# Optimization experiments

Hardware: AMD Instinct MI355X
Metric: run time of the kernel (lower is better)

## Reference

```python
import jax, jax.numpy as jnp
import numpy as np

NUM_ITEMS = 50000
B = 512      # batch of (user, item) pairs
L = 50       # padded per-user item-list length
K = 20       # top_k: length of each context channel
H = 32       # hidden_dim
D = 32       # output_dim


def setup_inputs() -> dict:
    key = jax.random.key(0)
    ks = jax.random.split(key, 8)
    ctx = jax.random.normal(ks[0], (NUM_ITEMS, 10, K), dtype=jnp.float32)
    item_idxs = jax.random.randint(ks[1], (B,), 0, NUM_ITEMS)
    user_items = jax.random.randint(ks[2], (B, L), 0, NUM_ITEMS)
    user_lens = jax.random.randint(ks[3], (B,), 1, L + 1)  # ragged lengths in [1, L]
    W1 = jax.random.normal(ks[4], (5, 1, H), dtype=jnp.float32) * 0.1
    b1 = jnp.zeros((5, H), dtype=jnp.float32)
    W2 = jax.random.normal(ks[5], (5, H, D), dtype=jnp.float32) * 0.1
    b2 = jnp.zeros((5, D), dtype=jnp.float32)
    Wout = jax.random.normal(ks[6], (D, 1), dtype=jnp.float32) * 0.1
    bout = jnp.zeros((1,), dtype=jnp.float32)
    return dict(ctx=ctx, W1=W1, b1=b1, W2=W2, b2=b2, Wout=Wout, bout=bout,
                item_idxs=item_idxs, user_items=user_items, user_lens=user_lens)


def _item_rep(feat, W1, b1, W2, b2):
    """feat: [..., 10, K] context channels -> [..., 5*K, D] item representation.
    Channels (2c, 2c+1) go through com_{c+1}: a shared 1->H->D MLP applied to each
    scalar (unsqueeze(1) in the original), outputs of the two channels multiplied."""
    prefix = feat.shape[:-2]
    x = feat.reshape(prefix + (5, 2, K))                     # [..., 5, 2, K]
    w1 = W1[:, 0, :].reshape((5, 1, 1, H))                   # input_dim == 1
    h = jax.nn.relu(x[..., None] * w1 + b1.reshape((5, 1, 1, H)))   # [..., 5, 2, K, H]
    o = jnp.einsum('...cpkh,chd->...cpkd', h, W2) + b2.reshape((5, 1, 1, D))
    rep = o[..., 0, :, :] * o[..., 1, :, :]                  # [..., 5, K, D]
    return rep.reshape(prefix + (5 * K, D))


def reference(ctx, W1, b1, W2, b2, Wout, bout, item_idxs, user_items, user_lens):
    # Target-item representations: gather contexts then tiny MLPs. [B, 5K, D]
    item_rep = _item_rep(ctx[item_idxs], W1, b1, W2, b2)
    # Per-user item reps (padded ragged) and masked mean over the item list.
    u_rep = _item_rep(ctx[user_items], W1, b1, W2, b2)       # [B, L, 5K, D]
    mask = (jnp.arange(L)[None, :] < user_lens[:, None]).astype(u_rep.dtype)  # [B, L]
    u_mean = jnp.einsum('blnd,bl->bnd', u_rep, mask) / user_lens[:, None, None].astype(u_rep.dtype)
    inter = u_mean * item_rep                                # [B, 5K, D]
    pred = jax.nn.sigmoid(inter @ Wout + bout)               # [B, 5K, 1]
    return pred.reshape(B * 5 * K, 1)
```

## Files before the change

kernel.cpp:

```cpp
#include <hip/hip_runtime.h>
#include <math.h>

#define NITEMS 50000
#define BATCH  512
#define LLEN   50
#define KTOP   20
#define HDIM   32
#define DDIM   32
#define NCH    5
#define NSEG   33
#define NSCAL  200
#define NCELL  100
#define THRP   33
#define NWAVE  8
#define CSLOT  13

typedef _Float16 h2 __attribute__((ext_vector_type(2)));

static __device__ __forceinline__ float dot2_acc(h2 a, h2 b, float c) {
#if __has_builtin(__builtin_amdgcn_fdot2)
    return __builtin_amdgcn_fdot2(a, b, c, false);
#else
    return fmaf((float)a.x, (float)b.x, fmaf((float)a.y, (float)b.y, c));
#endif
}

#define WS_THRS  0
#define WS_AB16  160
#define WS_ORDER 5440


__global__ __launch_bounds__(256) void cnn_setup(
        const float* __restrict__ W1, const float* __restrict__ b1,
        const float* __restrict__ W2, const float* __restrict__ b2,
        const int* __restrict__ user_lens,
        float* __restrict__ ws, int* __restrict__ order) {
    const int tid = threadIdx.x;

    if (blockIdx.x < NSEG) {
        __shared__ float sW1[NCH*HDIM], sB1[NCH*HDIM], sThr[NCH*HDIM];
        __shared__ int   sRank[NCH*HDIM];
        __shared__ float sW2[NCH*HDIM*DDIM];
        __shared__ float sB2[NCH*DDIM];

        for (int i = tid; i < NCH*HDIM; i += 256) { sW1[i] = W1[i]; sB1[i] = b1[i]; }
        for (int i = tid; i < NCH*HDIM*DDIM; i += 256) sW2[i] = W2[i];
        for (int i = tid; i < NCH*DDIM; i += 256) sB2[i] = b2[i];
        __syncthreads();

        for (int i = tid; i < NCH*HDIM; i += 256) {
            float w = sW1[i];
            sThr[i] = (w != 0.f) ? (-sB1[i] / w) : INFINITY;
        }
        __syncthreads();

        for (int i = tid; i < NCH*HDIM; i += 256) {
            int c = i / HDIM, h = i % HDIM;
            float thr = sThr[i];
            int rank = 0;
            for (int h2i = 0; h2i < HDIM; ++h2i) {
                float thr2 = sThr[c*HDIM + h2i];
                rank += (thr2 < thr || (thr2 == thr && h2i < h)) ? 1 : 0;
            }
            sRank[i] = rank;
            if (blockIdx.x == 0) ws[WS_THRS + c*HDIM + rank] = thr;
        }
        __syncthreads();

        const int s = blockIdx.x;
        if (tid < NCH*DDIM) {
            int c = tid / DDIM, d = tid % DDIM;
            float A = 0.f, Bv = 0.f;
#pragma unroll
            for (int h = 0; h < HDIM; ++h) {
                float w  = sW1[c*HDIM + h];
                float bb = sB1[c*HDIM + h];
                int   r  = sRank[c*HDIM + h];
                bool active = (w > 0.f) ? (r < s) : ((w < 0.f) ? (r >= s) : (bb > 0.f));
                if (active) {
                    float w2 = sW2[(c*HDIM + h)*DDIM + d];
                    A  = fmaf(w,  w2, A);
                    Bv = fmaf(bb, w2, Bv);
                }
            }
            Bv += sB2[c*DDIM + d];
            unsigned short* ab = (unsigned short*)(ws + WS_AB16);
            int d4 = d >> 2, dd = d & 3;
            int base = ((c*NSEG + s)*32 + d4*4)*2;
            _Float16 ah = (_Float16)A, bh = (_Float16)Bv;
            ab[base + 4*(dd>>1) + (dd&1)]     = __builtin_bit_cast(unsigned short, ah);
            ab[base + 4*(dd>>1) + 2 + (dd&1)] = __builtin_bit_cast(unsigned short, bh);
        }
    } else {
        __shared__ int k512[BATCH], v512[BATCH];
        for (int i = tid; i < BATCH; i += 256) { k512[i] = user_lens[i]; v512[i] = i; }
        __syncthreads();
        for (int k = 2; k <= BATCH; k <<= 1) {
            for (int j = k >> 1; j > 0; j >>= 1) {
                int i   = ((tid & ~(j - 1)) << 1) | (tid & (j - 1));
                int ixj = i | j;
                bool up = ((i & k) == 0);
                int ka = k512[i], kb = k512[ixj];
                if ((ka > kb) == up) {
                    k512[i] = kb; k512[ixj] = ka;
                    int va = v512[i]; v512[i] = v512[ixj]; v512[ixj] = va;
                }
                __syncthreads();
            }
        }
        for (int i = tid; i < BATCH; i += 256) order[i] = v512[i];
    }
}

__global__ __launch_bounds__(512, 4) void cnn_main(
        const float* __restrict__ ctx,  const float* __restrict__ ws,
        const float* __restrict__ Wout, const float* __restrict__ bout,
        const int* __restrict__ item_idxs, const int* __restrict__ user_items,
        const int* __restrict__ user_lens, const int* __restrict__ order,
        float* __restrict__ out) {
    __shared__ unsigned int sAB16[NCH*NSEG*32];
    __shared__ float  sThrS[NCH*THRP];
    __shared__ float4 sxo[NWAVE][NCELL];
    __shared__ union WScr {
        float rawx[NSCAL];
        float pRed[NCELL];
    } wscr[NWAVE];

    const int tid  = threadIdx.x;
    const int w    = tid >> 6;
    const int lane = tid & 63;
    const int g    = lane >> 3;
    const int d4   = lane & 7;

    const uint4* ABg = reinterpret_cast<const uint4*>(ws + WS_AB16);
    uint4* sAB4 = reinterpret_cast<uint4*>(sAB16);
    for (int i = tid; i < NCH*NSEG*8; i += 512) sAB4[i] = ABg[i];
    for (int i = tid; i < NCH*THRP; i += 512) {
        int c = i / THRP, j = i - c*THRP;
        sThrS[i] = (j < HDIM) ? ws[WS_THRS + c*HDIM + j] : 0.f;
    }

    const int rank = (blockIdx.x < 256) ? blockIdx.x : (767 - blockIdx.x);
    const int b    = order[rank];
    const int len  = user_lens[b];
    const float inv_len = 1.f / (float)len;
    const float bo = bout[0];
    const h2 wv0 = {(_Float16)Wout[4*d4],     (_Float16)Wout[4*d4 + 1]};
    const h2 wv1 = {(_Float16)Wout[4*d4 + 2], (_Float16)Wout[4*d4 + 3]};

    int sc[4], sdx[4], sdo[4];
#pragma unroll
    for (int r = 0; r < 4; ++r) {
        int idx  = lane + 64*r;
        int c    = idx / 40, rr = idx - c*40;
        int cell = c*KTOP + (rr % KTOP);
        int p    = rr / KTOP;
        sc[r]  = c;
        sdx[r] = cell*16 + p*4;
        sdo[r] = cell*16 + 8 + p*2;
    }

    const int nstripe = (len > w) ? ((len - w + NWAVE - 1) / NWAVE) : 0;

    unsigned int wtA[CSLOT], wtB[CSLOT];
    float acc[CSLOT];
#pragma unroll
    for (int i = 0; i < CSLOT; ++i) acc[i] = 0.f;

    __syncthreads();

    char* sxoB = (char*)&sxo[w][0];

    float4 x4 = make_float4(0.f, 0.f, 0.f, 0.f);
    {
        int it0 = item_idxs[b];
        if (lane < 50) x4 = *((const float4*)(ctx + (size_t)it0*NSCAL) + lane);
    }
    if (lane < 50) *((float4*)&wscr[w].rawx[0] + lane) = x4;
    __builtin_amdgcn_wave_barrier();

#pragma unroll
    for (int r = 0; r < 4; ++r) {
        int idx = lane + 64*r;
        if (idx < NSCAL) {
            float xv = wscr[w].rawx[idx];
            int base = sc[r]*THRP;
            int pos = 0;
            pos += (sThrS[base + pos + 15] < xv) ? 16 : 0;
            pos += (sThrS[base + pos + 7]  < xv) ? 8  : 0;
            pos += (sThrS[base + pos + 3]  < xv) ? 4  : 0;
            pos += (sThrS[base + pos + 1]  < xv) ? 2  : 0;
            pos += (sThrS[base + pos]      < xv) ? 1  : 0;
            int off = (sc[r]*NSEG + pos) << 7;
            *(float*)(sxoB + sdx[r]) = xv;
            *(unsigned short*)(sxoB + sdo[r]) = (unsigned short)off;
        }
    }
    __builtin_amdgcn_wave_barrier();

    float4 xn4 = make_float4(0.f, 0.f, 0.f, 0.f);
    if (nstripe > 0) {
        int nit = user_items[b*LLEN + w];
        if (lane < 50) xn4 = *((const float4*)(ctx + (size_t)nit*NSCAL) + lane);
    }

#pragma unroll
    for (int i = 0; i < CSLOT; ++i) {
        int cell = g + 8*i;
        if (cell < NCELL) {
            float4 xo = sxo[w][cell];
            unsigned int offs = __builtin_bit_cast(unsigned int, xo.z);
            const uint4* p0 = (const uint4*)((const char*)sAB16 + (offs & 0xffffu) + (d4 << 4));
            const uint4* p1 = (const uint4*)((const char*)sAB16 + (offs >> 16)     + (d4 << 4));
            uint4 q0 = *p0, q1 = *p1;
            _Float16 x0h = (_Float16)xo.x, x1h = (_Float16)xo.y;
            h2 x0 = {x0h, x0h}, x1 = {x1h, x1h};
            h2 repa = (x0 * __builtin_bit_cast(h2, q0.x) + __builtin_bit_cast(h2, q0.y))
                    * (x1 * __builtin_bit_cast(h2, q1.x) + __builtin_bit_cast(h2, q1.y));
            h2 repb = (x0 * __builtin_bit_cast(h2, q0.z) + __builtin_bit_cast(h2, q0.w))
                    * (x1 * __builtin_bit_cast(h2, q1.z) + __builtin_bit_cast(h2, q1.w));
            wtA[i] = __builtin_bit_cast(unsigned int, (h2)(repa * wv0));
            wtB[i] = __builtin_bit_cast(unsigned int, (h2)(repb * wv1));
        }
    }
    __builtin_amdgcn_wave_barrier();
    x4 = xn4;

    for (int j = 0; j < nstripe; ++j) {
        if (lane < 50) *((float4*)&wscr[w].rawx[0] + lane) = x4;
        __builtin_amdgcn_wave_barrier();

        xn4 = make_float4(0.f, 0.f, 0.f, 0.f);
        if (j + 1 < nstripe) {
            int nit = user_items[b*LLEN + w + NWAVE*(j + 1)];
            if (lane < 50) xn4 = *((const float4*)(ctx + (size_t)nit*NSCAL) + lane);
        }

#pragma unroll
        for (int r = 0; r < 4; ++r) {
            int idx = lane + 64*r;
            if (idx < NSCAL) {
                float xv = wscr[w].rawx[idx];
                int base = sc[r]*THRP;
                int pos = 0;
                pos += (sThrS[base + pos + 15] < xv) ? 16 : 0;
                pos += (sThrS[base + pos + 7]  < xv) ? 8  : 0;
                pos += (sThrS[base + pos + 3]  < xv) ? 4  : 0;
                pos += (sThrS[base + pos + 1]  < xv) ? 2  : 0;
                pos += (sThrS[base + pos]      < xv) ? 1  : 0;
                int off = (sc[r]*NSEG + pos) << 7;
                *(float*)(sxoB + sdx[r]) = xv;
                *(unsigned short*)(sxoB + sdo[r]) = (unsigned short)off;
            }
        }
        __builtin_amdgcn_wave_barrier();

#pragma unroll
        for (int i = 0; i < CSLOT; ++i) {
            int cell = g + 8*i;
            if (cell < NCELL) {
                float4 xo = sxo[w][cell];
                unsigned int offs = __builtin_bit_cast(unsigned int, xo.z);
                const uint4* p0 = (const uint4*)((const char*)sAB16 + (offs & 0xffffu) + (d4 << 4));
                const uint4* p1 = (const uint4*)((const char*)sAB16 + (offs >> 16)     + (d4 << 4));
                uint4 q0 = *p0, q1 = *p1;
                _Float16 x0h = (_Float16)xo.x, x1h = (_Float16)xo.y;
                h2 x0 = {x0h, x0h}, x1 = {x1h, x1h};
                h2 repa = (x0 * __builtin_bit_cast(h2, q0.x) + __builtin_bit_cast(h2, q0.y))
                        * (x1 * __builtin_bit_cast(h2, q1.x) + __builtin_bit_cast(h2, q1.y));
                h2 repb = (x0 * __builtin_bit_cast(h2, q0.z) + __builtin_bit_cast(h2, q0.w))
                        * (x1 * __builtin_bit_cast(h2, q1.z) + __builtin_bit_cast(h2, q1.w));
                acc[i] = dot2_acc(repa, __builtin_bit_cast(h2, wtA[i]),
                         dot2_acc(repb, __builtin_bit_cast(h2, wtB[i]), acc[i]));
            }
        }
        __builtin_amdgcn_wave_barrier();
        x4 = xn4;
    }

#pragma unroll
    for (int i = 0; i < CSLOT; ++i) {
        int cell = g + 8*i;
        float v = acc[i];
        v += __shfl_xor(v, 1, 64);
        v += __shfl_xor(v, 2, 64);
        v += __shfl_xor(v, 4, 64);
        if (d4 == 0 && cell < NCELL) wscr[w].pRed[cell] = v;
    }
    __syncthreads();
    if (tid < NCELL) {
        float p = 0.f;
#pragma unroll
        for (int q = 0; q < NWAVE; ++q) p += wscr[q].pRed[tid];
        out[b*NCELL + tid] = 1.f / (1.f + expf(-(p*inv_len + bo)));
    }
}

extern "C" void kernel_launch(void* const* d_in, const int* in_sizes, int n_in,
                              void* d_out, int out_size, void* d_ws, size_t ws_size,
                              hipStream_t stream) {
    const float* ctx   = (const float*)d_in[0];
    const float* W1    = (const float*)d_in[1];
    const float* b1    = (const float*)d_in[2];
    const float* W2    = (const float*)d_in[3];
    const float* b2    = (const float*)d_in[4];
    const float* Wout  = (const float*)d_in[5];
    const float* bout  = (const float*)d_in[6];
    const int* item_idxs  = (const int*)d_in[7];
    const int* user_items = (const int*)d_in[8];
    const int* user_lens  = (const int*)d_in[9];
    float* out = (float*)d_out;
    float* ws  = (float*)d_ws;
    int*   order = (int*)(ws + WS_ORDER);

    cnn_setup<<<NSEG + 1, 256, 0, stream>>>(W1, b1, W2, b2, user_lens, ws, order);
    cnn_main<<<BATCH, 512, 0, stream>>>(ctx, ws, Wout, bout,
                                        item_idxs, user_items, user_lens,
                                        order, out);
}
```

Before: 132.4 us.

## Compute target-item weights once per block and share via LDS

```diff
diff --git a/kernel.cpp b/kernel.cpp
--- a/kernel.cpp
+++ b/kernel.cpp
@@ -120,11 +120,9 @@
         float* __restrict__ out) {
     __shared__ unsigned int sAB16[NCH*NSEG*32];
     __shared__ float  sThrS[NCH*THRP];
-    __shared__ float4 sxo[NWAVE][NCELL];
-    __shared__ union WScr {
-        float rawx[NSCAL];
-        float pRed[NCELL];
-    } wscr[NWAVE];
+    __shared__ uint2  sxo[NWAVE][NCELL];
+    __shared__ uint2  sWt[NCELL*8];
+    __shared__ float  pRed[NWAVE][NCELL];
 
     const int tid  = threadIdx.x;
     const int w    = tid >> 6;
@@ -148,16 +146,14 @@
     const h2 wv0 = {(_Float16)Wout[4*d4],     (_Float16)Wout[4*d4 + 1]};
     const h2 wv1 = {(_Float16)Wout[4*d4 + 2], (_Float16)Wout[4*d4 + 3]};
 
-    int sc[4], sdx[4], sdo[4];
+    int sc[4], sdst[4];
 #pragma unroll
     for (int r = 0; r < 4; ++r) {
         int idx  = lane + 64*r;
         int c    = idx / 40, rr = idx - c*40;
         int cell = c*KTOP + (rr % KTOP);
-        int p    = rr / KTOP;
-        sc[r]  = c;
-        sdx[r] = cell*16 + p*4;
-        sdo[r] = cell*16 + 8 + p*2;
+        sc[r]   = c;
+        sdst[r] = cell*8 + (rr / KTOP)*4;
     }
 
     const int nstripe = (len > w) ? ((len - w + NWAVE - 1) / NWAVE) : 0;
@@ -167,80 +163,33 @@
 #pragma unroll
     for (int i = 0; i < CSLOT; ++i) acc[i] = 0.f;
 
+    char* sxoB = (char*)&sxo[w][0];
+
     __syncthreads();
 
-    char* sxoB = (char*)&sxo[w][0];
-
-    float4 x4 = make_float4(0.f, 0.f, 0.f, 0.f);
-    {
-        int it0 = item_idxs[b];
-        if (lane < 50) x4 = *((const float4*)(ctx + (size_t)it0*NSCAL) + lane);
-    }
-    if (lane < 50) *((float4*)&wscr[w].rawx[0] + lane) = x4;
-    __builtin_amdgcn_wave_barrier();
-
-#pragma unroll
-    for (int r = 0; r < 4; ++r) {
-        int idx = lane + 64*r;
-        if (idx < NSCAL) {
-            float xv = wscr[w].rawx[idx];
-            int base = sc[r]*THRP;
-            int pos = 0;
-            pos += (sThrS[base + pos + 15] < xv) ? 16 : 0;
-            pos += (sThrS[base + pos + 7]  < xv) ? 8  : 0;
-            pos += (sThrS[base + pos + 3]  < xv) ? 4  : 0;
-            pos += (sThrS[base + pos + 1]  < xv) ? 2  : 0;
-            pos += (sThrS[base + pos]      < xv) ? 1  : 0;
-            int off = (sc[r]*NSEG + pos) << 7;
-            *(float*)(sxoB + sdx[r]) = xv;
-            *(unsigned short*)(sxoB + sdo[r]) = (unsigned short)off;
-        }
-    }
-    __builtin_amdgcn_wave_barrier();
-
-    float4 xn4 = make_float4(0.f, 0.f, 0.f, 0.f);
+    float xp[4] = {0.f, 0.f, 0.f, 0.f};
     if (nstripe > 0) {
-        int nit = user_items[b*LLEN + w];
-        if (lane < 50) xn4 = *((const float4*)(ctx + (size_t)nit*NSCAL) + lane);
-    }
-
-#pragma unroll
-    for (int i = 0; i < CSLOT; ++i) {
-        int cell = g + 8*i;
-        if (cell < NCELL) {
-            float4 xo = sxo[w][cell];
-            unsigned int offs = __builtin_bit_cast(unsigned int, xo.z);
-            const uint4* p0 = (const uint4*)((const char*)sAB16 + (offs & 0xffffu) + (d4 << 4));
-            const uint4* p1 = (const uint4*)((const char*)sAB16 + (offs >> 16)     + (d4 << 4));
-            uint4 q0 = *p0, q1 = *p1;
-            _Float16 x0h = (_Float16)xo.x, x1h = (_Float16)xo.y;
-            h2 x0 = {x0h, x0h}, x1 = {x1h, x1h};
-            h2 repa = (x0 * __builtin_bit_cast(h2, q0.x) + __builtin_bit_cast(h2, q0.y))
-                    * (x1 * __builtin_bit_cast(h2, q1.x) + __builtin_bit_cast(h2, q1.y));
-            h2 repb = (x0 * __builtin_bit_cast(h2, q0.z) + __builtin_bit_cast(h2, q0.w))
-                    * (x1 * __builtin_bit_cast(h2, q1.z) + __builtin_bit_cast(h2, q1.w));
-            wtA[i] = __builtin_bit_cast(unsigned int, (h2)(repa * wv0));
-            wtB[i] = __builtin_bit_cast(unsigned int, (h2)(repb * wv1));
-        }
-    }
-    __builtin_amdgcn_wave_barrier();
-    x4 = xn4;
-
-    for (int j = 0; j < nstripe; ++j) {
-        if (lane < 50) *((float4*)&wscr[w].rawx[0] + lane) = x4;
-        __builtin_amdgcn_wave_barrier();
-
-        xn4 = make_float4(0.f, 0.f, 0.f, 0.f);
-        if (j + 1 < nstripe) {
-            int nit = user_items[b*LLEN + w + NWAVE*(j + 1)];
-            if (lane < 50) xn4 = *((const float4*)(ctx + (size_t)nit*NSCAL) + lane);
-        }
-
+        const float* row = ctx + (size_t)user_items[b*LLEN + w] * NSCAL;
+#pragma unroll
+        for (int r = 0; r < 4; ++r) {
+            int idx = lane + 64*r;
+            if (idx < NSCAL) xp[r] = row[idx];
+        }
+    }
+
+    if (w == 0) {
+        float xt[4] = {0.f, 0.f, 0.f, 0.f};
+        const float* row = ctx + (size_t)item_idxs[b] * NSCAL;
+#pragma unroll
+        for (int r = 0; r < 4; ++r) {
+            int idx = lane + 64*r;
+            if (idx < NSCAL) xt[r] = row[idx];
+        }
 #pragma unroll
         for (int r = 0; r < 4; ++r) {
             int idx = lane + 64*r;
             if (idx < NSCAL) {
-                float xv = wscr[w].rawx[idx];
+                float xv = xt[r];
                 int base = sc[r]*THRP;
                 int pos = 0;
                 pos += (sThrS[base + pos + 15] < xv) ? 16 : 0;
@@ -248,23 +197,93 @@
                 pos += (sThrS[base + pos + 3]  < xv) ? 4  : 0;
                 pos += (sThrS[base + pos + 1]  < xv) ? 2  : 0;
                 pos += (sThrS[base + pos]      < xv) ? 1  : 0;
-                int off = (sc[r]*NSEG + pos) << 7;
-                *(float*)(sxoB + sdx[r]) = xv;
-                *(unsigned short*)(sxoB + sdo[r]) = (unsigned short)off;
+                unsigned int off = (unsigned int)((sc[r]*NSEG + pos) << 7);
+                _Float16 xh = (_Float16)xv;
+                unsigned int word = (unsigned int)__builtin_bit_cast(unsigned short, xh)
+                                  | (off << 16);
+                *(unsigned int*)(sxoB + sdst[r]) = word;
             }
         }
         __builtin_amdgcn_wave_barrier();
-
 #pragma unroll
         for (int i = 0; i < CSLOT; ++i) {
             int cell = g + 8*i;
             if (cell < NCELL) {
-                float4 xo = sxo[w][cell];
-                unsigned int offs = __builtin_bit_cast(unsigned int, xo.z);
-                const uint4* p0 = (const uint4*)((const char*)sAB16 + (offs & 0xffffu) + (d4 << 4));
-                const uint4* p1 = (const uint4*)((const char*)sAB16 + (offs >> 16)     + (d4 << 4));
+                uint2 xo = sxo[0][cell];
+                const uint4* p0 = (const uint4*)((const char*)sAB16 + (xo.x >> 16) + (d4 << 4));
+                const uint4* p1 = (const uint4*)((const char*)sAB16 + (xo.y >> 16) + (d4 << 4));
                 uint4 q0 = *p0, q1 = *p1;
-                _Float16 x0h = (_Float16)xo.x, x1h = (_Float16)xo.y;
+                _Float16 x0h = __builtin_bit_cast(_Float16, (unsigned short)(xo.x & 0xffffu));
+                _Float16 x1h = __builtin_bit_cast(_Float16, (unsigned short)(xo.y & 0xffffu));
+                h2 x0 = {x0h, x0h}, x1 = {x1h, x1h};
+                h2 repa = (x0 * __builtin_bit_cast(h2, q0.x) + __builtin_bit_cast(h2, q0.y))
+                        * (x1 * __builtin_bit_cast(h2, q1.x) + __builtin_bit_cast(h2, q1.y));
+                h2 repb = (x0 * __builtin_bit_cast(h2, q0.z) + __builtin_bit_cast(h2, q0.w))
+                        * (x1 * __builtin_bit_cast(h2, q1.z) + __builtin_bit_cast(h2, q1.w));
+                wtA[i] = __builtin_bit_cast(unsigned int, (h2)(repa * wv0));
+                wtB[i] = __builtin_bit_cast(unsigned int, (h2)(repb * wv1));
+                sWt[cell*8 + d4] = make_uint2(wtA[i], wtB[i]);
+            }
+        }
+    }
+    __syncthreads();
+
+    if (w != 0) {
+#pragma unroll
+        for (int i = 0; i < CSLOT; ++i) {
+            int cell = g + 8*i;
+            if (cell < NCELL) {
+                uint2 v = sWt[cell*8 + d4];
+                wtA[i] = v.x; wtB[i] = v.y;
+            }
+        }
+    }
+
+    for (int j = 0; j < nstripe; ++j) {
+        float xc[4];
+#pragma unroll
+        for (int r = 0; r < 4; ++r) xc[r] = xp[r];
+
+        if (j + 1 < nstripe) {
+            const float* row = ctx + (size_t)user_items[b*LLEN + w + NWAVE*(j+1)] * NSCAL;
+#pragma unroll
+            for (int r = 0; r < 4; ++r) {
+                int idx = lane + 64*r;
+                if (idx < NSCAL) xp[r] = row[idx];
+            }
+        }
+
+#pragma unroll
+        for (int r = 0; r < 4; ++r) {
+            int idx = lane + 64*r;
+            if (idx < NSCAL) {
+                float xv = xc[r];
+                int base = sc[r]*THRP;
+                int pos = 0;
+                pos += (sThrS[base + pos + 15] < xv) ? 16 : 0;
+                pos += (sThrS[base + pos + 7]  < xv) ? 8  : 0;
+                pos += (sThrS[base + pos + 3]  < xv) ? 4  : 0;
+                pos += (sThrS[base + pos + 1]  < xv) ? 2  : 0;
+                pos += (sThrS[base + pos]      < xv) ? 1  : 0;
+                unsigned int off = (unsigned int)((sc[r]*NSEG + pos) << 7);
+                _Float16 xh = (_Float16)xv;
+                unsigned int word = (unsigned int)__builtin_bit_cast(unsigned short, xh)
+                                  | (off << 16);
+                *(unsigned int*)(sxoB + sdst[r]) = word;
+            }
+        }
+        __builtin_amdgcn_wave_barrier();
+
+#pragma unroll
+        for (int i = 0; i < CSLOT; ++i) {
+            int cell = g + 8*i;
+            if (cell < NCELL) {
+                uint2 xo = sxo[w][cell];
+                const uint4* p0 = (const uint4*)((const char*)sAB16 + (xo.x >> 16) + (d4 << 4));
+                const uint4* p1 = (const uint4*)((const char*)sAB16 + (xo.y >> 16) + (d4 << 4));
+                uint4 q0 = *p0, q1 = *p1;
+                _Float16 x0h = __builtin_bit_cast(_Float16, (unsigned short)(xo.x & 0xffffu));
+                _Float16 x1h = __builtin_bit_cast(_Float16, (unsigned short)(xo.y & 0xffffu));
                 h2 x0 = {x0h, x0h}, x1 = {x1h, x1h};
                 h2 repa = (x0 * __builtin_bit_cast(h2, q0.x) + __builtin_bit_cast(h2, q0.y))
                         * (x1 * __builtin_bit_cast(h2, q1.x) + __builtin_bit_cast(h2, q1.y));
@@ -275,7 +294,6 @@
             }
         }
         __builtin_amdgcn_wave_barrier();
-        x4 = xn4;
     }
 
 #pragma unroll
@@ -285,13 +303,13 @@
         v += __shfl_xor(v, 1, 64);
         v += __shfl_xor(v, 2, 64);
         v += __shfl_xor(v, 4, 64);
-        if (d4 == 0 && cell < NCELL) wscr[w].pRed[cell] = v;
+        if (d4 == 0 && cell < NCELL) pRed[w][cell] = v;
     }
     __syncthreads();
     if (tid < NCELL) {
         float p = 0.f;
 #pragma unroll
-        for (int q = 0; q < NWAVE; ++q) p += wscr[q].pRed[tid];
+        for (int q = 0; q < NWAVE; ++q) p += pRed[q][tid];
         out[b*NCELL + tid] = 1.f / (1.f + expf(-(p*inv_len + bo)));
     }
 }
```

Measured after the change: 115.3 us. 12.9% less time.
